# Kernel optimization log

Measured on AMD Instinct MI355X. Metric: run time of the kernel, lower is better.

Reference implementation:

```python
import jax, jax.numpy as jnp
import numpy as np

H = 1024      # hidden_size
NH = 16       # n_heads
DK = 64       # d_kv


def setup_inputs() -> dict:
    key = jax.random.key(0)
    k1, k2, k3, k4, k5 = jax.random.split(key, 5)
    x = jax.random.normal(k1, (4, 2048, H), dtype=jnp.float32)
    # dense1: hidden -> 3*n_heads*d_kv
    W1 = jax.random.normal(k2, (H, 3 * NH * DK), dtype=jnp.float32) / np.sqrt(H)
    b1 = jax.random.normal(k3, (3 * NH * DK,), dtype=jnp.float32) * 0.02
    # dense2: n_heads*d_kv -> hidden
    W2 = jax.random.normal(k4, (NH * DK, H), dtype=jnp.float32) / np.sqrt(NH * DK)
    b2 = jax.random.normal(k5, (H,), dtype=jnp.float32) * 0.02
    return {"x": x, "W1": W1, "b1": b1, "W2": W2, "b2": b2}


def reference(x, W1, b1, W2, b2):
    B, S, _ = x.shape
    scale = 1.0 / np.sqrt(DK)
    qkv = x @ W1 + b1                                   # [B,S,3*NH*DK]
    qkv = qkv.reshape(B, S, 3, NH, DK)
    q, k, v = jnp.moveaxis(qkv, 2, 0)                   # each [B,S,NH,DK]
    q = q.transpose(0, 2, 1, 3)                         # [B,NH,S,DK]
    k = k.transpose(0, 2, 1, 3)
    v = v.transpose(0, 2, 1, 3)
    scores = jnp.einsum('bhqd,bhkd->bhqk', q, k) * scale  # [B,NH,S,S]
    attn = jax.nn.softmax(scores, axis=-1)
    ctx = jnp.einsum('bhqk,bhkd->bhqd', attn, v)        # [B,NH,S,DK]
    ctx = ctx.transpose(0, 2, 1, 3).reshape(B, S, NH * DK)
    return ctx @ W2 + b2
```

## Files before the change

### kernel.cpp

```cpp
#include <hip/hip_runtime.h>
#include <hip/hip_bf16.h>


typedef __hip_bfloat16 bf16;
typedef __attribute__((ext_vector_type(8))) short bf16x8;
typedef __attribute__((ext_vector_type(4))) float f32x4;

#define B_   4
#define S_   2048
#define H_   1024
#define NH_  16
#define DK_  64
#define M_   8192
#define N1_  3072
#define K_   1024

#define SCALE_Q 0.18033688f

typedef const __attribute__((address_space(1))) void* gas_t;
typedef __attribute__((address_space(3))) void* las_t;
#define G2L16(g, l) __builtin_amdgcn_global_load_lds((gas_t)(g), (las_t)(l), 16, 0, 0)

__device__ __forceinline__ float b2f(bf16 v) { return __bfloat162float(v); }

__device__ __forceinline__ unsigned pk2(float a, float b) {
    unsigned ua = __float_as_uint(a);
    unsigned ub = __float_as_uint(b);
    ua += 0x7FFFu + ((ua >> 16) & 1u);
    ub += 0x7FFFu + ((ub >> 16) & 1u);
    return (ua >> 16) | (ub & 0xFFFF0000u);
}

__global__ __launch_bounds__(256) void conv_x(const float* __restrict__ X,
                                              bf16* __restrict__ Xb)
{
    size_t i = ((size_t)blockIdx.x * 256 + threadIdx.x) * 8;
    float4 lo = *(const float4*)&X[i];
    float4 hi = *(const float4*)&X[i + 4];
    uint4 u;
    u.x = pk2(lo.x, lo.y); u.y = pk2(lo.z, lo.w);
    u.z = pk2(hi.x, hi.y); u.w = pk2(hi.z, hi.w);
    *(uint4*)&Xb[i] = u;
}

__global__ __launch_bounds__(256) void conv_wT(const float* __restrict__ W,
                                               bf16* __restrict__ WT,
                                               int Kdim, int Ndim)
{
    __shared__ bf16 T[64][72];
    const int tid = threadIdx.x;
    const int n0 = blockIdx.x * 64, k0 = blockIdx.y * 64;
    const int kr = tid >> 4, nc = (tid & 15) * 4;
    #pragma unroll
    for (int p = 0; p < 4; ++p) {
        float4 v = *(const float4*)&W[(size_t)(k0 + kr + p * 16) * Ndim + n0 + nc];
        T[nc + 0][kr + p * 16] = __float2bfloat16(v.x);
        T[nc + 1][kr + p * 16] = __float2bfloat16(v.y);
        T[nc + 2][kr + p * 16] = __float2bfloat16(v.z);
        T[nc + 3][kr + p * 16] = __float2bfloat16(v.w);
    }
    __syncthreads();
    const int nr = tid >> 2, kc = (tid & 3) * 16;
    *(bf16x8*)&WT[(size_t)(n0 + nr) * Kdim + k0 + kc]     = *(const bf16x8*)&T[nr][kc];
    *(bf16x8*)&WT[(size_t)(n0 + nr) * Kdim + k0 + kc + 8] = *(const bf16x8*)&T[nr][kc + 8];
}

__device__ __forceinline__ void qkv_epilogue(
    const f32x4 acc[4][4], const float* __restrict__ B1,
    bf16* __restrict__ Qp, bf16* __restrict__ Kp, bf16* __restrict__ Vt,
    int n0, int m0, int wm, int wn, int quad, int col)
{
    const int which = n0 >> 10;
    const int bb = m0 >> 11;
    if (which == 2) {
        #pragma unroll
        for (int i = 0; i < 4; ++i) {
            int s = (m0 & (S_ - 1)) + wm * 64 + i * 16 + quad * 4;
            #pragma unroll
            for (int j = 0; j < 4; ++j) {
                int n = n0 + wn * 64 + j * 16 + col;
                int h = (n >> 6) & 15, d = n & 63;
                float bv = B1[n];
                uint2 t;
                t.x = pk2(acc[i][j][0] + bv, acc[i][j][1] + bv);
                t.y = pk2(acc[i][j][2] + bv, acc[i][j][3] + bv);
                *(uint2*)&Vt[(((size_t)(bb * NH_ + h)) * DK_ + d) * S_ + s] = t;
            }
        }
    } else {
        bf16* dst = which ? Kp : Qp;
        const float sc = which ? 1.0f : SCALE_Q;
        #pragma unroll
        for (int i = 0; i < 4; ++i) {
            #pragma unroll
            for (int r = 0; r < 4; ++r) {
                int s = (m0 & (S_ - 1)) + wm * 64 + i * 16 + quad * 4 + r;
                #pragma unroll
                for (int j = 0; j < 4; ++j) {
                    int n = n0 + wn * 64 + j * 16 + col;
                    int h = (n >> 6) & 15, d = n & 63;
                    dst[(((size_t)(bb * NH_ + h)) * S_ + s) * DK_ + d] =
                        __float2bfloat16((acc[i][j][r] + B1[n]) * sc);
                }
            }
        }
    }
}

__global__ __launch_bounds__(256) void gemm_qkv_mfma2(
    const bf16* __restrict__ Xb, const bf16* __restrict__ W1T,
    const float* __restrict__ B1,
    bf16* __restrict__ Qp, bf16* __restrict__ Kp, bf16* __restrict__ Vt)
{
    __shared__ bf16 As[128 * 32];
    __shared__ bf16 Bs[128 * 32];

    const int tid = threadIdx.x;
    const int lane = tid & 63, wv = tid >> 6;
    const int col = lane & 15, quad = lane >> 4;
    const int wm = wv >> 1, wn = wv & 1;
    const int n0 = blockIdx.x * 128, m0 = blockIdx.y * 128;

    f32x4 acc[4][4] = {};

    const bf16* Ag = Xb  + (size_t)m0 * K_;
    const bf16* Bg = W1T + (size_t)n0 * K_;

    for (int k0 = 0; k0 < K_; k0 += 32) {
        #pragma unroll
        for (int h = 0; h < 2; ++h) {
            int idx = tid + h * 256;
            int row = idx >> 2, c = (idx & 3) * 8;
            G2L16(Ag + (size_t)row * K_ + k0 + c, As + (size_t)idx * 8);
            G2L16(Bg + (size_t)row * K_ + k0 + c, Bs + (size_t)idx * 8);
        }
        __syncthreads();

        bf16x8 af[4], bfr[4];
        #pragma unroll
        for (int i = 0; i < 4; ++i)
            af[i] = *(const bf16x8*)&As[(wm * 64 + i * 16 + col) * 32 + quad * 8];
        #pragma unroll
        for (int j = 0; j < 4; ++j)
            bfr[j] = *(const bf16x8*)&Bs[(wn * 64 + j * 16 + col) * 32 + quad * 8];

        #pragma unroll
        for (int i = 0; i < 4; ++i)
            #pragma unroll
            for (int j = 0; j < 4; ++j)
                acc[i][j] = __builtin_amdgcn_mfma_f32_16x16x32_bf16(af[i], bfr[j], acc[i][j], 0, 0, 0);
        __syncthreads();
    }
    qkv_epilogue(acc, B1, Qp, Kp, Vt, n0, m0, wm, wn, quad, col);
}

__global__ __launch_bounds__(256) void gemm_qkv_mfma(
    const float* __restrict__ X, const bf16* __restrict__ W1T,
    const float* __restrict__ B1,
    bf16* __restrict__ Qp, bf16* __restrict__ Kp, bf16* __restrict__ Vt)
{
    __shared__ bf16 As[128 * 32];
    __shared__ bf16 Bs[128 * 32];

    const int tid = threadIdx.x;
    const int lane = tid & 63, wv = tid >> 6;
    const int col = lane & 15, quad = lane >> 4;
    const int wm = wv >> 1, wn = wv & 1;
    const int n0 = blockIdx.x * 128, m0 = blockIdx.y * 128;

    f32x4 acc[4][4] = {};

    const float* Ag = X   + (size_t)m0 * K_;
    const bf16*  Bg = W1T + (size_t)n0 * K_;

    for (int k0 = 0; k0 < K_; k0 += 32) {
        #pragma unroll
        for (int h = 0; h < 2; ++h) {
            int idx = tid + h * 256;
            int row = idx >> 2, c = (idx & 3) * 8;
            G2L16(Bg + (size_t)row * K_ + k0 + c, Bs + (size_t)idx * 8);
        }
        #pragma unroll
        for (int h = 0; h < 2; ++h) {
            int idx = tid + h * 256;
            int row = idx >> 2, c = (idx & 3) * 8;
            float4 lo = *(const float4*)&Ag[(size_t)row * K_ + k0 + c];
            float4 hi = *(const float4*)&Ag[(size_t)row * K_ + k0 + c + 4];
            uint4 u;
            u.x = pk2(lo.x, lo.y); u.y = pk2(lo.z, lo.w);
            u.z = pk2(hi.x, hi.y); u.w = pk2(hi.z, hi.w);
            *(uint4*)&As[(size_t)idx * 8] = u;
        }
        __syncthreads();

        bf16x8 af[4], bfr[4];
        #pragma unroll
        for (int i = 0; i < 4; ++i)
            af[i] = *(const bf16x8*)&As[(wm * 64 + i * 16 + col) * 32 + quad * 8];
        #pragma unroll
        for (int j = 0; j < 4; ++j)
            bfr[j] = *(const bf16x8*)&Bs[(wn * 64 + j * 16 + col) * 32 + quad * 8];

        #pragma unroll
        for (int i = 0; i < 4; ++i)
            #pragma unroll
            for (int j = 0; j < 4; ++j)
                acc[i][j] = __builtin_amdgcn_mfma_f32_16x16x32_bf16(af[i], bfr[j], acc[i][j], 0, 0, 0);
        __syncthreads();
    }
    qkv_epilogue(acc, B1, Qp, Kp, Vt, n0, m0, wm, wn, quad, col);
}

__global__ __launch_bounds__(512, 8) void attn_mfma(
    const bf16* __restrict__ Q, const bf16* __restrict__ K,
    const bf16* __restrict__ Vt, bf16* __restrict__ CTX)
{
    __shared__ bf16 Ks[64][72];
    __shared__ bf16 Vs[64][72];
    __shared__ bf16 Ps[8][16][72];

    const int tid  = threadIdx.x;
    const int wv   = tid >> 6;
    const int lane = tid & 63;
    const int col  = lane & 15;
    const int quad = lane >> 4;

    const int bh = blockIdx.y;
    const int q0 = blockIdx.x * 128;

    const bf16* Qg  = Q  + (size_t)bh * S_ * DK_;
    const bf16* Kg  = K  + (size_t)bh * S_ * DK_;
    const bf16* Vtg = Vt + (size_t)bh * DK_ * S_;

    const short oneb = (short)0x3F80;
    const bf16x8 ones = {oneb, oneb, oneb, oneb, oneb, oneb, oneb, oneb};

    const int qrow = q0 + wv * 16 + col;
    bf16x8 qf[2];
    qf[0] = *(const bf16x8*)&Qg[(size_t)qrow * DK_ + quad * 8];
    qf[1] = *(const bf16x8*)&Qg[(size_t)qrow * DK_ + 32 + quad * 8];

    f32x4 o[4] = {};
    f32x4 l_acc = {0.f, 0.f, 0.f, 0.f};

    const int sr = tid >> 3;
    const int e0 = (tid & 7) * 8;

    bf16x8 kreg = *(const bf16x8*)&Kg[(size_t)sr * DK_ + e0];
    bf16x8 vreg = *(const bf16x8*)&Vtg[(size_t)sr * S_ + e0];

    for (int kt = 0; kt < S_ / 64; ++kt) {
        *(bf16x8*)&Ks[sr][e0] = kreg;
        *(bf16x8*)&Vs[sr][e0] = vreg;
        __syncthreads();

        if (kt + 1 < S_ / 64) {
            kreg = *(const bf16x8*)&Kg[(size_t)((kt + 1) * 64 + sr) * DK_ + e0];
            vreg = *(const bf16x8*)&Vtg[(size_t)sr * S_ + (kt + 1) * 64 + e0];
        }

        #pragma unroll
        for (int cs = 0; cs < 4; ++cs) {
            const bf16* kb = &Ks[cs * 16 + col][0];
            f32x4 a = {0.f, 0.f, 0.f, 0.f};
            a = __builtin_amdgcn_mfma_f32_16x16x32_bf16(*(const bf16x8*)&kb[quad * 8],      qf[0], a, 0, 0, 0);
            a = __builtin_amdgcn_mfma_f32_16x16x32_bf16(*(const bf16x8*)&kb[32 + quad * 8], qf[1], a, 0, 0, 0);
            uint2 p;
            p.x = pk2(exp2f(a[0]), exp2f(a[1]));
            p.y = pk2(exp2f(a[2]), exp2f(a[3]));
            *(uint2*)&Ps[wv][col][cs * 16 + quad * 4] = p;
        }

        bf16x8 pf0 = *(const bf16x8*)&Ps[wv][col][quad * 8];
        bf16x8 pf1 = *(const bf16x8*)&Ps[wv][col][32 + quad * 8];

        l_acc = __builtin_amdgcn_mfma_f32_16x16x32_bf16(ones, pf0, l_acc, 0, 0, 0);
        l_acc = __builtin_amdgcn_mfma_f32_16x16x32_bf16(ones, pf1, l_acc, 0, 0, 0);

        #pragma unroll
        for (int ds = 0; ds < 4; ++ds) {
            const bf16* vb = &Vs[ds * 16 + col][0];
            o[ds] = __builtin_amdgcn_mfma_f32_16x16x32_bf16(*(const bf16x8*)&vb[quad * 8],      pf0, o[ds], 0, 0, 0);
            o[ds] = __builtin_amdgcn_mfma_f32_16x16x32_bf16(*(const bf16x8*)&vb[32 + quad * 8], pf1, o[ds], 0, 0, 0);
        }
        __syncthreads();
    }

    const int b = bh >> 4, h = bh & 15;
    const float inv = 1.f / l_acc[0];
    const int srow = q0 + wv * 16 + col;
    bf16* crow = CTX + ((size_t)(b * S_ + srow)) * H_ + h * DK_;
    #pragma unroll
    for (int ds = 0; ds < 4; ++ds) {
        uint2 t;
        t.x = pk2(o[ds][0] * inv, o[ds][1] * inv);
        t.y = pk2(o[ds][2] * inv, o[ds][3] * inv);
        *(uint2*)&crow[ds * 16 + quad * 4] = t;
    }
}

__global__ __launch_bounds__(256) void gemm_out_mfma(
    const bf16* __restrict__ Cx, const bf16* __restrict__ W2T,
    const float* __restrict__ B2, float* __restrict__ OUT)
{
    __shared__ bf16 As[128 * 32];
    __shared__ bf16 Bs[128 * 32];

    const int tid = threadIdx.x;
    const int lane = tid & 63, wv = tid >> 6;
    const int col = lane & 15, quad = lane >> 4;
    const int wm = wv >> 1, wn = wv & 1;
    const int n0 = blockIdx.x * 128, m0 = blockIdx.y * 128;

    f32x4 acc[4][4] = {};

    const bf16* Ag = Cx  + (size_t)m0 * K_;
    const bf16* Bg = W2T + (size_t)n0 * K_;

    for (int k0 = 0; k0 < K_; k0 += 32) {
        #pragma unroll
        for (int h = 0; h < 2; ++h) {
            int idx = tid + h * 256;
            int row = idx >> 2, c = (idx & 3) * 8;
            G2L16(Ag + (size_t)row * K_ + k0 + c, As + (size_t)idx * 8);
            G2L16(Bg + (size_t)row * K_ + k0 + c, Bs + (size_t)idx * 8);
        }
        __syncthreads();

        bf16x8 af[4], bfr[4];
        #pragma unroll
        for (int i = 0; i < 4; ++i)
            af[i] = *(const bf16x8*)&As[(wm * 64 + i * 16 + col) * 32 + quad * 8];
        #pragma unroll
        for (int j = 0; j < 4; ++j)
            bfr[j] = *(const bf16x8*)&Bs[(wn * 64 + j * 16 + col) * 32 + quad * 8];

        #pragma unroll
        for (int i = 0; i < 4; ++i)
            #pragma unroll
            for (int j = 0; j < 4; ++j)
                acc[i][j] = __builtin_amdgcn_mfma_f32_16x16x32_bf16(af[i], bfr[j], acc[i][j], 0, 0, 0);
        __syncthreads();
    }

    #pragma unroll
    for (int i = 0; i < 4; ++i) {
        #pragma unroll
        for (int r = 0; r < 4; ++r) {
            int m = m0 + wm * 64 + i * 16 + quad * 4 + r;
            #pragma unroll
            for (int j = 0; j < 4; ++j) {
                int n = n0 + wn * 64 + j * 16 + col;
                OUT[(size_t)m * H_ + n] = acc[i][j][r] + B2[n];
            }
        }
    }
}

extern "C" void kernel_launch(void* const* d_in, const int* in_sizes, int n_in,
                              void* d_out, int out_size, void* d_ws, size_t ws_size,
                              hipStream_t stream)
{
    const float* X  = (const float*)d_in[0];
    const float* W1 = (const float*)d_in[1];
    const float* B1 = (const float*)d_in[2];
    const float* W2 = (const float*)d_in[3];
    const float* B2 = (const float*)d_in[4];
    float* OUT = (float*)d_out;

    const size_t QE = (size_t)B_ * NH_ * S_ * DK_;
    bf16* Qw  = (bf16*)d_ws;
    bf16* Kw  = Qw + QE;
    bf16* Vw  = Kw + QE;
    bf16* Rw  = Vw + QE;
    bf16* W1T = Rw;
    bf16* Cw  = Rw;
    bf16* W2T = Qw;
    bf16* Xb  = Rw + QE;

    const bool fast = ws_size >= 5 * QE * sizeof(bf16);

    conv_wT<<<dim3(N1_ / 64, K_ / 64), 256, 0, stream>>>(W1, W1T, K_, N1_);
    if (fast) {
        conv_x<<<dim3((int)(QE / (256 * 8))), 256, 0, stream>>>(X, Xb);
        gemm_qkv_mfma2<<<dim3(N1_ / 128, M_ / 128), 256, 0, stream>>>(Xb, W1T, B1, Qw, Kw, Vw);
    } else {
        gemm_qkv_mfma<<<dim3(N1_ / 128, M_ / 128), 256, 0, stream>>>(X, W1T, B1, Qw, Kw, Vw);
    }
    attn_mfma<<<dim3(S_ / 128, B_ * NH_), 512, 0, stream>>>(Qw, Kw, Vw, Cw);
    conv_wT<<<dim3(H_ / 64, K_ / 64), 256, 0, stream>>>(W2, W2T, K_, H_);
    gemm_out_mfma<<<dim3(H_ / 128, M_ / 128), 256, 0, stream>>>(Cw, W2T, B2, OUT);
}
```

Baseline: 318.0 us.

## Drop LDS staging of K/V in attention; load directly with 32 query rows per wave

The attention kernel no longer stages K and V tiles through shared memory with block-wide barriers. Each wave now reads K and V fragments straight from global memory (relying on cache) and handles two 16-row query tiles, so each K/V fragment is reused across 32 queries. The block shrinks to 256 threads, and only the per-wave P buffer stays in LDS, which removes both __syncthreads per tile. The tradeoff is more global/L2 traffic with uncoalesced-ish per-lane loads and higher register pressure from the doubled accumulators.

```diff
diff --git a/kernel.cpp b/kernel.cpp
--- a/kernel.cpp
+++ b/kernel.cpp
@@ -211,13 +211,11 @@
     qkv_epilogue(acc, B1, Qp, Kp, Vt, n0, m0, wm, wn, quad, col);
 }
 
-__global__ __launch_bounds__(512, 8) void attn_mfma(
+__global__ __launch_bounds__(256, 4) void attn_mfma(
     const bf16* __restrict__ Q, const bf16* __restrict__ K,
     const bf16* __restrict__ Vt, bf16* __restrict__ CTX)
 {
-    __shared__ bf16 Ks[64][72];
-    __shared__ bf16 Vs[64][72];
-    __shared__ bf16 Ps[8][16][72];
+    __shared__ bf16 Ps[4][32][72];
 
     const int tid  = threadIdx.x;
     const int wv   = tid >> 6;
@@ -235,67 +233,84 @@
     const short oneb = (short)0x3F80;
     const bf16x8 ones = {oneb, oneb, oneb, oneb, oneb, oneb, oneb, oneb};
 
-    const int qrow = q0 + wv * 16 + col;
-    bf16x8 qf[2];
-    qf[0] = *(const bf16x8*)&Qg[(size_t)qrow * DK_ + quad * 8];
-    qf[1] = *(const bf16x8*)&Qg[(size_t)qrow * DK_ + 32 + quad * 8];
-
-    f32x4 o[4] = {};
-    f32x4 l_acc = {0.f, 0.f, 0.f, 0.f};
-
-    const int sr = tid >> 3;
-    const int e0 = (tid & 7) * 8;
-
-    bf16x8 kreg = *(const bf16x8*)&Kg[(size_t)sr * DK_ + e0];
-    bf16x8 vreg = *(const bf16x8*)&Vtg[(size_t)sr * S_ + e0];
+    bf16x8 qf[2][2];
+    #pragma unroll
+    for (int rt = 0; rt < 2; ++rt) {
+        const int qrow = q0 + wv * 32 + rt * 16 + col;
+        qf[rt][0] = *(const bf16x8*)&Qg[(size_t)qrow * DK_ + quad * 8];
+        qf[rt][1] = *(const bf16x8*)&Qg[(size_t)qrow * DK_ + 32 + quad * 8];
+    }
+
+    f32x4 o[2][4] = {};
+    f32x4 l_acc[2] = {f32x4{0,0,0,0}, f32x4{0,0,0,0}};
 
     for (int kt = 0; kt < S_ / 64; ++kt) {
-        *(bf16x8*)&Ks[sr][e0] = kreg;
-        *(bf16x8*)&Vs[sr][e0] = vreg;
-        __syncthreads();
-
-        if (kt + 1 < S_ / 64) {
-            kreg = *(const bf16x8*)&Kg[(size_t)((kt + 1) * 64 + sr) * DK_ + e0];
-            vreg = *(const bf16x8*)&Vtg[(size_t)sr * S_ + (kt + 1) * 64 + e0];
-        }
-
+        const bf16* Kt = Kg + (size_t)(kt * 64) * DK_;
+
+        f32x4 s[2][4];
         #pragma unroll
         for (int cs = 0; cs < 4; ++cs) {
-            const bf16* kb = &Ks[cs * 16 + col][0];
-            f32x4 a = {0.f, 0.f, 0.f, 0.f};
-            a = __builtin_amdgcn_mfma_f32_16x16x32_bf16(*(const bf16x8*)&kb[quad * 8],      qf[0], a, 0, 0, 0);
-            a = __builtin_amdgcn_mfma_f32_16x16x32_bf16(*(const bf16x8*)&kb[32 + quad * 8], qf[1], a, 0, 0, 0);
-            uint2 p;
-            p.x = pk2(exp2f(a[0]), exp2f(a[1]));
-            p.y = pk2(exp2f(a[2]), exp2f(a[3]));
-            *(uint2*)&Ps[wv][col][cs * 16 + quad * 4] = p;
-        }
-
-        bf16x8 pf0 = *(const bf16x8*)&Ps[wv][col][quad * 8];
-        bf16x8 pf1 = *(const bf16x8*)&Ps[wv][col][32 + quad * 8];
-
-        l_acc = __builtin_amdgcn_mfma_f32_16x16x32_bf16(ones, pf0, l_acc, 0, 0, 0);
-        l_acc = __builtin_amdgcn_mfma_f32_16x16x32_bf16(ones, pf1, l_acc, 0, 0, 0);
-
+            const bf16* kr = &Kt[(size_t)(cs * 16 + col) * DK_];
+            bf16x8 k0 = *(const bf16x8*)&kr[quad * 8];
+            bf16x8 k1 = *(const bf16x8*)&kr[32 + quad * 8];
+            #pragma unroll
+            for (int rt = 0; rt < 2; ++rt) {
+                f32x4 a = {0.f, 0.f, 0.f, 0.f};
+                a = __builtin_amdgcn_mfma_f32_16x16x32_bf16(k0, qf[rt][0], a, 0, 0, 0);
+                a = __builtin_amdgcn_mfma_f32_16x16x32_bf16(k1, qf[rt][1], a, 0, 0, 0);
+                s[rt][cs] = a;
+            }
+        }
+
+        #pragma unroll
+        for (int rt = 0; rt < 2; ++rt)
+            #pragma unroll
+            for (int cs = 0; cs < 4; ++cs) {
+                uint2 p;
+                p.x = pk2(exp2f(s[rt][cs][0]), exp2f(s[rt][cs][1]));
+                p.y = pk2(exp2f(s[rt][cs][2]), exp2f(s[rt][cs][3]));
+                *(uint2*)&Ps[wv][rt * 16 + col][cs * 16 + quad * 4] = p;
+            }
+
+        bf16x8 vf[4][2];
         #pragma unroll
         for (int ds = 0; ds < 4; ++ds) {
-            const bf16* vb = &Vs[ds * 16 + col][0];
-            o[ds] = __builtin_amdgcn_mfma_f32_16x16x32_bf16(*(const bf16x8*)&vb[quad * 8],      pf0, o[ds], 0, 0, 0);
-            o[ds] = __builtin_amdgcn_mfma_f32_16x16x32_bf16(*(const bf16x8*)&vb[32 + quad * 8], pf1, o[ds], 0, 0, 0);
-        }
-        __syncthreads();
+            const bf16* vr = &Vtg[(size_t)(ds * 16 + col) * S_ + kt * 64];
+            vf[ds][0] = *(const bf16x8*)&vr[quad * 8];
+            vf[ds][1] = *(const bf16x8*)&vr[32 + quad * 8];
+        }
+
+        bf16x8 pf[2][2];
+        #pragma unroll
+        for (int rt = 0; rt < 2; ++rt) {
+            pf[rt][0] = *(const bf16x8*)&Ps[wv][rt * 16 + col][quad * 8];
+            pf[rt][1] = *(const bf16x8*)&Ps[wv][rt * 16 + col][32 + quad * 8];
+            l_acc[rt] = __builtin_amdgcn_mfma_f32_16x16x32_bf16(ones, pf[rt][0], l_acc[rt], 0, 0, 0);
+            l_acc[rt] = __builtin_amdgcn_mfma_f32_16x16x32_bf16(ones, pf[rt][1], l_acc[rt], 0, 0, 0);
+        }
+
+        #pragma unroll
+        for (int ds = 0; ds < 4; ++ds)
+            #pragma unroll
+            for (int rt = 0; rt < 2; ++rt) {
+                o[rt][ds] = __builtin_amdgcn_mfma_f32_16x16x32_bf16(vf[ds][0], pf[rt][0], o[rt][ds], 0, 0, 0);
+                o[rt][ds] = __builtin_amdgcn_mfma_f32_16x16x32_bf16(vf[ds][1], pf[rt][1], o[rt][ds], 0, 0, 0);
+            }
     }
 
     const int b = bh >> 4, h = bh & 15;
-    const float inv = 1.f / l_acc[0];
-    const int srow = q0 + wv * 16 + col;
-    bf16* crow = CTX + ((size_t)(b * S_ + srow)) * H_ + h * DK_;
     #pragma unroll
-    for (int ds = 0; ds < 4; ++ds) {
-        uint2 t;
-        t.x = pk2(o[ds][0] * inv, o[ds][1] * inv);
-        t.y = pk2(o[ds][2] * inv, o[ds][3] * inv);
-        *(uint2*)&crow[ds * 16 + quad * 4] = t;
+    for (int rt = 0; rt < 2; ++rt) {
+        const float inv = 1.f / l_acc[rt][0];
+        const int srow = q0 + wv * 32 + rt * 16 + col;
+        bf16* crow = CTX + ((size_t)(b * S_ + srow)) * H_ + h * DK_;
+        #pragma unroll
+        for (int ds = 0; ds < 4; ++ds) {
+            uint2 t;
+            t.x = pk2(o[rt][ds][0] * inv, o[rt][ds][1] * inv);
+            t.y = pk2(o[rt][ds][2] * inv, o[rt][ds][3] * inv);
+            *(uint2*)&crow[ds * 16 + quad * 4] = t;
+        }
     }
 }
 
@@ -387,7 +402,7 @@
     } else {
         gemm_qkv_mfma<<<dim3(N1_ / 128, M_ / 128), 256, 0, stream>>>(X, W1T, B1, Qw, Kw, Vw);
     }
-    attn_mfma<<<dim3(S_ / 128, B_ * NH_), 512, 0, stream>>>(Qw, Kw, Vw, Cw);
+    attn_mfma<<<dim3(S_ / 128, B_ * NH_), 256, 0, stream>>>(Qw, Kw, Vw, Cw);
     conv_wT<<<dim3(H_ / 64, K_ / 64), 256, 0, stream>>>(W2, W2T, K_, H_);
     gemm_out_mfma<<<dim3(H_ / 128, M_ / 128), 256, 0, stream>>>(Cw, W2T, B2, OUT);
 }
```

After: 454.3 us. 42.9% more time.
